# Performance work log

Measured on AMD Instinct MI355X. Metric: run time of the kernel, lower is better.

## Reference

```python
import jax, jax.numpy as jnp
import numpy as np

N = 40000   # nodes
E = 600000  # edges
G = 64      # graphs
DIN = 128   # input feature dim
H = 128     # hidden_channels
L = 3       # num_layers


def setup_inputs() -> dict:
    key = jax.random.key(0)
    ks = jax.random.split(key, 16)
    s = 0.05
    inp = {}
    inp["x"] = jax.random.normal(ks[0], (N, DIN), jnp.float32)
    inp["edge_attr"] = jax.random.normal(ks[1], (E,), jnp.float32)
    inp["node_w"] = jax.random.normal(ks[2], (DIN, H), jnp.float32) * s
    inp["node_b"] = jnp.zeros((H,), jnp.float32)
    inp["edge_w"] = jax.random.normal(ks[3], (1, H), jnp.float32) * s
    inp["edge_b"] = jnp.zeros((H,), jnp.float32)
    inp["t"] = jnp.ones((L,), jnp.float32)  # learn_t init 1.0
    inp["lin1_w"] = jax.random.normal(ks[4], (L, H, 2 * H), jnp.float32) * s
    inp["lin1_b"] = jnp.zeros((L, 2 * H), jnp.float32)
    inp["ln1_g"] = jnp.ones((L, 2 * H), jnp.float32)
    inp["ln1_bt"] = jnp.zeros((L, 2 * H), jnp.float32)
    inp["lin2_w"] = jax.random.normal(ks[5], (L, 2 * H, H), jnp.float32) * s
    inp["lin2_b"] = jnp.zeros((L, H), jnp.float32)
    inp["blk_g"] = jnp.ones((L, H), jnp.float32)
    inp["blk_b"] = jnp.zeros((L, H), jnp.float32)
    inp["hw1"] = jax.random.normal(ks[6], (H, H // 2), jnp.float32) * s
    inp["hb1"] = jnp.zeros((H // 2,), jnp.float32)
    inp["hw2"] = jax.random.normal(ks[7], (H // 2, H // 4), jnp.float32) * s
    inp["hb2"] = jnp.zeros((H // 4,), jnp.float32)
    inp["hw3"] = jax.random.normal(ks[8], (H // 4, 1), jnp.float32) * s
    inp["hb3"] = jnp.zeros((1,), jnp.float32)
    inp["edge_index"] = jax.random.randint(ks[9], (2, E), 0, N, jnp.int32)
    inp["batch"] = jnp.sort(jax.random.randint(ks[10], (N,), 0, G, jnp.int32))
    return inp


def _layer_norm(v, g, b):
    mu = jnp.mean(v, axis=-1, keepdims=True)
    var = jnp.var(v, axis=-1, keepdims=True)
    return (v - mu) * jax.lax.rsqrt(var + 1e-5) * g + b


def reference(x, edge_attr, node_w, node_b, edge_w, edge_b, t,
              lin1_w, lin1_b, ln1_g, ln1_bt, lin2_w, lin2_b,
              blk_g, blk_b, hw1, hb1, hw2, hb2, hw3, hb3,
              edge_index, batch):
    src, dst = edge_index[0], edge_index[1]
    h = x @ node_w + node_b                       # [N, H]
    ea = edge_attr[:, None] @ edge_w + edge_b     # [E, H]

    def genconv(xn, i):
        # message: relu(x_j + e) + eps
        msg = jax.nn.relu(xn[src] + ea) + 1e-7    # [E, H]
        # scatter-softmax over dst with learnable temperature t
        logit = msg * t[i]
        m = jax.ops.segment_max(logit, dst, num_segments=N)
        m = jnp.where(jnp.isfinite(m), m, 0.0)    # isolated nodes
        ex = jnp.exp(logit - m[dst])
        den = jax.ops.segment_sum(ex, dst, num_segments=N)
        agg = jax.ops.segment_sum(ex * msg, dst, num_segments=N) / jnp.maximum(den, 1e-16)
        o = agg + xn                              # add root
        # GENConv MLP: Linear(H,2H) -> LayerNorm -> ReLU -> Linear(2H,H)
        o = jax.nn.relu(_layer_norm(o @ lin1_w[i] + lin1_b[i], ln1_g[i], ln1_bt[i]))
        return o @ lin2_w[i] + lin2_b[i]

    # layer 0: bare conv (as in the torch forward)
    h = genconv(h, 0)
    # layers 1..L-1: DeepGCNLayer res+ (norm -> act -> [dropout=id in eval] -> conv -> residual)
    for i in range(1, L):
        r = jax.nn.relu(_layer_norm(h, blk_g[i], blk_b[i]))
        h = h + genconv(r, i)
    # final norm+act uses layer 0's norm/act
    h = jax.nn.relu(_layer_norm(h, blk_g[0], blk_b[0]))
    # global mean pool over graphs
    cnt = jax.ops.segment_sum(jnp.ones((N,), h.dtype), batch, num_segments=G)
    pooled = jax.ops.segment_sum(h, batch, num_segments=G) / jnp.maximum(cnt, 1.0)[:, None]
    # MLP head (dropout = identity in eval)
    o = jax.nn.relu(pooled @ hw1 + hb1)
    o = jax.nn.relu(o @ hw2 + hb2)
    return o @ hw3 + hb3                          # [G, 1]
```

## Files before the change

### kernel.cpp

```cpp
#include <hip/hip_runtime.h>
#include <math.h>

#define NN 40000
#define NE 600000
#define NG 64
#define DIM_IN 128
#define HH 128
#define HH2 256

using half8 = __attribute__((ext_vector_type(8))) _Float16;
using half4 = __attribute__((ext_vector_type(4))) _Float16;
using h2    = __attribute__((ext_vector_type(2))) _Float16;
using f4    = __attribute__((ext_vector_type(4))) float;

__device__ __forceinline__ int lower_bound_dev(const int* a, int n, int key) {
    int lo = 0, hi = n;
    while (lo < hi) { int mid = (lo + hi) >> 1; if (a[mid] < key) lo = mid + 1; else hi = mid; }
    return lo;
}

__global__ void convert_w_kernel(const float* __restrict__ node_w,
                                 const float* __restrict__ lin1_w, const float* __restrict__ lin2_w,
                                 _Float16* __restrict__ nwt,
                                 _Float16* __restrict__ w1t, _Float16* __restrict__ w2t)
{
    int id = blockIdx.x * blockDim.x + threadIdx.x;
    if (id < 16384) { int n = id >> 7, k = id & 127; nwt[id] = (_Float16)node_w[k*128 + n]; return; }
    id -= 16384;
    if (id < 98304) {
        int l = id >> 15, r = id & 32767;
        int n = r >> 7, k = r & 127;
        w1t[id] = (_Float16)lin1_w[l*32768 + k*256 + n];
        return;
    }
    id -= 98304;
    if (id < 98304) {
        int l = id >> 15, r = id & 32767;
        int n = r >> 8, k = r & 255;
        w2t[id] = (_Float16)lin2_w[l*32768 + k*128 + n];
    }
}

__global__ void count_rank_kernel(const int* __restrict__ dst, int* __restrict__ counts,
                                  int* __restrict__ rank) {
    int e = blockIdx.x * blockDim.x + threadIdx.x;
    if (e < NE) rank[e] = atomicAdd(&counts[dst[e]], 1);
}

__global__ __launch_bounds__(1024) void scanA_kernel(const int* __restrict__ counts,
                                                     int* __restrict__ tmp, int* __restrict__ btot) {
    __shared__ int wpre[16];
    int t = threadIdx.x, lane = t & 63, wid = t >> 6;
    int i = blockIdx.x * 1024 + t;
    int v = (i < NN) ? counts[i] : 0;
    int s = v;
    #pragma unroll
    for (int off = 1; off < 64; off <<= 1) {
        int u = __shfl_up(s, off, 64);
        if (lane >= off) s += u;
    }
    if (lane == 63) wpre[wid] = s;
    __syncthreads();
    if (t == 0) {
        int run = 0;
        #pragma unroll
        for (int j = 0; j < 16; ++j) { int xv = wpre[j]; wpre[j] = run; run += xv; }
        btot[blockIdx.x] = run;
    }
    __syncthreads();
    if (i < NN) tmp[i] = s + wpre[wid];
}

__global__ __launch_bounds__(64) void scanB_kernel(const int* __restrict__ btot,
                                                   int* __restrict__ boff, int nb) {
    int t = threadIdx.x;
    int v = (t < nb) ? btot[t] : 0;
    int s = v;
    #pragma unroll
    for (int off = 1; off < 64; off <<= 1) {
        int u = __shfl_up(s, off, 64);
        if (t >= off) s += u;
    }
    if (t < nb) boff[t] = s - v;
}

__global__ __launch_bounds__(1024) void scanC_kernel(const int* __restrict__ tmp,
                                                     const int* __restrict__ boff,
                                                     int* __restrict__ rowp) {
    int i = blockIdx.x * 1024 + threadIdx.x;
    if (i < NN) rowp[i + 1] = tmp[i] + boff[blockIdx.x];
    if (i == 0) rowp[0] = 0;
}

__global__ void fill2_kernel(const int* __restrict__ src, const int* __restrict__ dst,
                             const float* __restrict__ eattr, const int* __restrict__ rowp,
                             const int* __restrict__ rank, int2* __restrict__ rec) {
    int e = blockIdx.x * blockDim.x + threadIdx.x;
    if (e < NE) {
        int pos = rowp[dst[e]] + rank[e];
        rec[pos] = make_int2(src[e], __float_as_int(eattr[e]));
    }
}

__global__ __launch_bounds__(256) void agg_kernel(
    const _Float16* __restrict__ xh,
    const int* __restrict__ row_ptr,
    const int2* __restrict__ rec,
    const float* __restrict__ ew, const float* __restrict__ eb,
    const float* __restrict__ tptr, int layer,
    _Float16* __restrict__ oh)
{
    int d = blockIdx.x * 4 + (threadIdx.x >> 6);
    int lane = threadIdx.x & 63;
    int half = lane >> 5;
    int sl = lane & 31;
    int c0 = 4 * sl;
    float tc2 = tptr[layer] * 1.44269504f;
    float ewv[4], ebv[4];
    #pragma unroll
    for (int c = 0; c < 4; ++c) { ewv[c] = ew[c0 + c]; ebv[c] = eb[c0 + c]; }
    int beg = row_ptr[d], end = row_ptr[d + 1];
    float den[4] = {0.f, 0.f, 0.f, 0.f}, num[4] = {0.f, 0.f, 0.f, 0.f};
    for (int base = beg; base < end; base += 64) {
        int cnt = min(64, end - base);
        int2 mv = rec[base + min(lane, cnt - 1)];
        int sv = mv.x;
        float av = __int_as_float(mv.y);
        int pcnt = (cnt + 1) >> 1;
        half4 gA[4], gB[4]; float aA[4], aB[4];
        auto issue = [&](half4 (&g)[4], float (&aa)[4], int p0) {
            #pragma unroll
            for (int u = 0; u < 4; ++u) {
                int je = min(2 * (p0 + u) + half, cnt - 1);
                int s = __shfl(sv, je, 64);
                aa[u] = __shfl(av, je, 64);
                g[u] = *(const half4*)(xh + ((size_t)s << 7) + c0);
            }
        };
        auto consume = [&](half4 (&g)[4], float (&aa)[4], int p0) {
            #pragma unroll
            for (int u = 0; u < 4; ++u) {
                int je = 2 * (p0 + u) + half;
                if (je < cnt) {
                    #pragma unroll
                    for (int c = 0; c < 4; ++c) {
                        float r = fmaxf(__fmaf_rn(aa[u], ewv[c], ebv[c]) + (float)g[u][c], 0.f);
                        float e = exp2f(r * tc2);
                        den[c] += e;
                        num[c] = __fmaf_rn(e, r, num[c]);
                    }
                }
            }
        };
        issue(gA, aA, 0);
        for (int p0 = 0; p0 < pcnt; p0 += 8) {
            if (p0 + 4 < pcnt) issue(gB, aB, p0 + 4);
            consume(gA, aA, p0);
            if (p0 + 8 < pcnt) issue(gA, aA, p0 + 8);
            if (p0 + 4 < pcnt) consume(gB, aB, p0 + 4);
        }
    }
    #pragma unroll
    for (int c = 0; c < 4; ++c) {
        den[c] += __shfl_xor(den[c], 32, 64);
        num[c] += __shfl_xor(num[c], 32, 64);
    }
    if (half == 0) {
        half4 sv4 = *(const half4*)(xh + ((size_t)d << 7) + c0);
        half4 ov;
        #pragma unroll
        for (int c = 0; c < 4; ++c) {
            float o = num[c] / fmaxf(den[c], 1e-16f) + 1e-7f + (float)sv4[c];
            ov[c] = (_Float16)o;
        }
        *(half4*)(oh + ((size_t)d << 7) + c0) = ov;
    }
}

__global__ __launch_bounds__(256) void gemm_mfma(
    const float* __restrict__ A, const _Float16* __restrict__ Bt,
    const float* __restrict__ bias, _Float16* __restrict__ C,
    int M, int N, int K)
{
    constexpr int LDA = 40;
    __shared__ _Float16 As[64 * LDA];
    __shared__ _Float16 Bs[128 * LDA];
    int t = threadIdx.x;
    int row0 = blockIdx.y * 64;
    int col0 = blockIdx.x * 128;
    int w = t >> 6, lane = t & 63;
    int wm = w & 1, wn = w >> 1;
    int q = lane >> 4, l16 = lane & 15;
    f4 acc[2][4];
    #pragma unroll
    for (int i = 0; i < 2; ++i)
        #pragma unroll
        for (int j = 0; j < 4; ++j)
            acc[i][j] = (f4){0.f, 0.f, 0.f, 0.f};

    for (int k0 = 0; k0 < K; k0 += 32) {
        #pragma unroll
        for (int p = 0; p < 2; ++p) {
            int idx = t + p * 256;
            int r = idx >> 3, seg = idx & 7;
            float4 v = *(const float4*)(A + (size_t)(row0 + r) * K + k0 + seg * 4);
            half4 o; o.x = (_Float16)v.x; o.y = (_Float16)v.y; o.z = (_Float16)v.z; o.w = (_Float16)v.w;
            *(half4*)&As[r * LDA + seg * 4] = o;
        }
        #pragma unroll
        for (int i = 0; i < 2; ++i) {
            int idx = t + i * 256;
            int r = idx >> 2, seg = idx & 3;
            *(float4*)&Bs[r * LDA + seg * 8] =
                *(const float4*)(Bt + (size_t)(col0 + r) * K + k0 + seg * 8);
        }
        __syncthreads();
        half8 af[2], bf[4];
        #pragma unroll
        for (int i = 0; i < 2; ++i)
            af[i] = *(const half8*)&As[(wm * 32 + i * 16 + l16) * LDA + q * 8];
        #pragma unroll
        for (int j = 0; j < 4; ++j)
            bf[j] = *(const half8*)&Bs[(wn * 64 + j * 16 + l16) * LDA + q * 8];
        #pragma unroll
        for (int i = 0; i < 2; ++i)
            #pragma unroll
            for (int j = 0; j < 4; ++j)
                acc[i][j] = __builtin_amdgcn_mfma_f32_16x16x32_f16(af[i], bf[j], acc[i][j], 0, 0, 0);
        __syncthreads();
    }
    #pragma unroll
    for (int j = 0; j < 4; ++j) {
        int col = col0 + wn * 64 + j * 16 + l16;
        float bv = bias[col];
        #pragma unroll
        for (int i = 0; i < 2; ++i) {
            int rbase = row0 + wm * 32 + i * 16 + q * 4;
            #pragma unroll
            for (int rg = 0; rg < 4; ++rg)
                C[(size_t)(rbase + rg) * N + col] = (_Float16)(acc[i][j][rg] + bv);
        }
    }
}

template<int RES, int FINAL>
__global__ __launch_bounds__(256) void mlp_fused(
    const _Float16* __restrict__ Ain,
    const _Float16* __restrict__ w1t,
    const float* __restrict__ b1,
    const float* __restrict__ g1, const float* __restrict__ bt1,
    const _Float16* __restrict__ w2t,
    const float* __restrict__ b2,
    float* __restrict__ h,
    const float* __restrict__ bg, const float* __restrict__ bb,
    _Float16* __restrict__ xout)
{
    constexpr int LDA = 136;
    constexpr int LDB = 40;
    constexpr int LDM = 264;
    __shared__ _Float16 As[64 * LDA];
    __shared__ _Float16 Bs[256 * LDB];
    __shared__ _Float16 midh[64 * LDM];
    __shared__ float ssum[64][2], ssum2[64][2];
    int t = threadIdx.x;
    int row0 = blockIdx.x * 64;
    int w = t >> 6, lane = t & 63;
    int wm = w & 1, wn = w >> 1;
    int q = lane >> 4, l16 = lane & 15;

    #pragma unroll
    for (int p = 0; p < 4; ++p) {
        int idx = t + p * 256;
        int r = idx >> 4, seg = idx & 15;
        *(float4*)&As[r * LDA + seg * 8] =
            *(const float4*)(Ain + (size_t)(row0 + r) * 128 + seg * 8);
    }

    f4 acc[2][8];
    #pragma unroll
    for (int i = 0; i < 2; ++i)
        #pragma unroll
        for (int j = 0; j < 8; ++j)
            acc[i][j] = (f4){0.f, 0.f, 0.f, 0.f};
    for (int k0 = 0; k0 < 128; k0 += 32) {
        #pragma unroll
        for (int p = 0; p < 4; ++p) {
            int idx = t + p * 256;
            int r = idx >> 2, seg = idx & 3;
            *(float4*)&Bs[r * LDB + seg * 8] =
                *(const float4*)(w1t + (size_t)r * 128 + k0 + seg * 8);
        }
        __syncthreads();
        half8 af[2], bf[8];
        #pragma unroll
        for (int i = 0; i < 2; ++i)
            af[i] = *(const half8*)&As[(wm * 32 + i * 16 + l16) * LDA + k0 + q * 8];
        #pragma unroll
        for (int j = 0; j < 8; ++j)
            bf[j] = *(const half8*)&Bs[(wn * 128 + j * 16 + l16) * LDB + q * 8];
        #pragma unroll
        for (int i = 0; i < 2; ++i)
            #pragma unroll
            for (int j = 0; j < 8; ++j)
                acc[i][j] = __builtin_amdgcn_mfma_f32_16x16x32_f16(af[i], bf[j], acc[i][j], 0, 0, 0);
        __syncthreads();
    }

    float b1v[8], g1v[8], bt1v[8];
    #pragma unroll
    for (int j = 0; j < 8; ++j) {
        int col = wn * 128 + j * 16 + l16;
        b1v[j] = b1[col]; g1v[j] = g1[col]; bt1v[j] = bt1[col];
    }
    float vals[2][8][4];
    #pragma unroll
    for (int i = 0; i < 2; ++i)
        #pragma unroll
        for (int j = 0; j < 8; ++j)
            #pragma unroll
            for (int rg = 0; rg < 4; ++rg)
                vals[i][j][rg] = acc[i][j][rg] + b1v[j];
    #pragma unroll
    for (int i = 0; i < 2; ++i) {
        #pragma unroll
        for (int rg = 0; rg < 4; ++rg) {
            float ps = 0.f, ps2 = 0.f;
            #pragma unroll
            for (int j = 0; j < 8; ++j) { float v = vals[i][j][rg]; ps += v; ps2 += v * v; }
            #pragma unroll
            for (int off = 1; off < 16; off <<= 1) {
                ps  += __shfl_xor(ps,  off, 16);
                ps2 += __shfl_xor(ps2, off, 16);
            }
            if (l16 == 0) {
                int row = wm * 32 + i * 16 + q * 4 + rg;
                ssum[row][wn] = ps; ssum2[row][wn] = ps2;
            }
        }
    }
    __syncthreads();
    #pragma unroll
    for (int i = 0; i < 2; ++i) {
        #pragma unroll
        for (int rg = 0; rg < 4; ++rg) {
            int row = wm * 32 + i * 16 + q * 4 + rg;
            float S = ssum[row][0] + ssum[row][1];
            float S2 = ssum2[row][0] + ssum2[row][1];
            float mu = S * (1.0f / 256.0f);
            float var = S2 * (1.0f / 256.0f) - mu * mu;
            float rstd = rsqrtf(var + 1e-5f);
            #pragma unroll
            for (int j = 0; j < 8; ++j) {
                int col = wn * 128 + j * 16 + l16;
                float o = fmaxf((vals[i][j][rg] - mu) * rstd * g1v[j] + bt1v[j], 0.f);
                midh[row * LDM + col] = (_Float16)o;
            }
        }
    }
    __syncthreads();

    f4 acc2[2][4];
    #pragma unroll
    for (int i = 0; i < 2; ++i)
        #pragma unroll
        for (int j = 0; j < 4; ++j)
            acc2[i][j] = (f4){0.f, 0.f, 0.f, 0.f};
    for (int k0 = 0; k0 < 256; k0 += 32) {
        #pragma unroll
        for (int p = 0; p < 2; ++p) {
            int idx = t + p * 256;
            int r = idx >> 2, seg = idx & 3;
            *(float4*)&Bs[r * LDB + seg * 8] =
                *(const float4*)(w2t + (size_t)r * 256 + k0 + seg * 8);
        }
        __syncthreads();
        half8 af2[2], bf2[4];
        #pragma unroll
        for (int i = 0; i < 2; ++i)
            af2[i] = *(const half8*)&midh[(wm * 32 + i * 16 + l16) * LDM + k0 + q * 8];
        #pragma unroll
        for (int j = 0; j < 4; ++j)
            bf2[j] = *(const half8*)&Bs[(wn * 64 + j * 16 + l16) * LDB + q * 8];
        #pragma unroll
        for (int i = 0; i < 2; ++i)
            #pragma unroll
            for (int j = 0; j < 4; ++j)
                acc2[i][j] = __builtin_amdgcn_mfma_f32_16x16x32_f16(af2[i], bf2[j], acc2[i][j], 0, 0, 0);
        __syncthreads();
    }

    float b2v[4], bgv[4], bbv[4];
    #pragma unroll
    for (int j = 0; j < 4; ++j) {
        int col = wn * 64 + j * 16 + l16;
        b2v[j] = b2[col]; bgv[j] = bg[col]; bbv[j] = bb[col];
    }
    float ov[2][4][4];
    #pragma unroll
    for (int i = 0; i < 2; ++i) {
        #pragma unroll
        for (int rg = 0; rg < 4; ++rg) {
            int row = wm * 32 + i * 16 + q * 4 + rg;
            #pragma unroll
            for (int j = 0; j < 4; ++j) {
                int col = wn * 64 + j * 16 + l16;
                float v = acc2[i][j][rg] + b2v[j];
                size_t gidx = (size_t)(row0 + row) * 128 + col;
                if (RES) v += h[gidx];
                if (!FINAL) h[gidx] = v;
                ov[i][j][rg] = v;
            }
        }
    }
    #pragma unroll
    for (int i = 0; i < 2; ++i) {
        #pragma unroll
        for (int rg = 0; rg < 4; ++rg) {
            float ps = 0.f, ps2 = 0.f;
            #pragma unroll
            for (int j = 0; j < 4; ++j) { float v = ov[i][j][rg]; ps += v; ps2 += v * v; }
            #pragma unroll
            for (int off = 1; off < 16; off <<= 1) {
                ps  += __shfl_xor(ps,  off, 16);
                ps2 += __shfl_xor(ps2, off, 16);
            }
            if (l16 == 0) {
                int row = wm * 32 + i * 16 + q * 4 + rg;
                ssum[row][wn] = ps; ssum2[row][wn] = ps2;
            }
        }
    }
    __syncthreads();
    #pragma unroll
    for (int i = 0; i < 2; ++i) {
        #pragma unroll
        for (int rg = 0; rg < 4; ++rg) {
            int row = wm * 32 + i * 16 + q * 4 + rg;
            float S = ssum[row][0] + ssum[row][1];
            float S2 = ssum2[row][0] + ssum2[row][1];
            float mu = S * (1.0f / 128.0f);
            float var = S2 * (1.0f / 128.0f) - mu * mu;
            float rstd = rsqrtf(var + 1e-5f);
            #pragma unroll
            for (int j = 0; j < 4; ++j) {
                int col = wn * 64 + j * 16 + l16;
                float o = fmaxf((ov[i][j][rg] - mu) * rstd * bgv[j] + bbv[j], 0.f);
                xout[(size_t)(row0 + row) * 128 + col] = (_Float16)o;
            }
        }
    }
}

__global__ __launch_bounds__(128) void pool_kernel(
    const _Float16* __restrict__ f, const int* __restrict__ batch, float* __restrict__ pooled)
{
    int g = blockIdx.x;
    int chunk = blockIdx.y;
    int c = threadIdx.x;
    int s = lower_bound_dev(batch, NN, g);
    int e = lower_bound_dev(batch, NN, g + 1);
    int len = e - s;
    if (len <= 0) return;
    int nch = gridDim.y;
    int per = (len + nch - 1) / nch;
    int cs = s + chunk * per;
    int ce = min(cs + per, e);
    if (cs >= ce) return;
    float acc = 0.f;
    for (int n = cs; n < ce; ++n) acc += (float)f[(size_t)n * HH + c];
    atomicAdd(&pooled[g * HH + c], acc);
}

__global__ __launch_bounds__(128) void head_kernel(
    const float* __restrict__ pooled, const int* __restrict__ batch,
    const float* __restrict__ hw1, const float* __restrict__ hb1,
    const float* __restrict__ hw2, const float* __restrict__ hb2,
    const float* __restrict__ hw3, const float* __restrict__ hb3,
    float* __restrict__ out)
{
    __shared__ float p[HH];
    __shared__ float o1[64];
    __shared__ float o2[32];
    int g = blockIdx.x;
    int t = threadIdx.x;
    int s = lower_bound_dev(batch, NN, g);
    int e = lower_bound_dev(batch, NN, g + 1);
    float cnt = fmaxf((float)(e - s), 1.0f);
    p[t] = pooled[g * HH + t] / cnt;
    __syncthreads();
    if (t < 64) {
        float acc = hb1[t];
        for (int k = 0; k < HH; ++k) acc += p[k] * hw1[k * 64 + t];
        o1[t] = fmaxf(acc, 0.f);
    }
    __syncthreads();
    if (t < 32) {
        float acc = hb2[t];
        for (int k = 0; k < 64; ++k) acc += o1[k] * hw2[k * 32 + t];
        o2[t] = fmaxf(acc, 0.f);
    }
    __syncthreads();
    if (t == 0) {
        float acc = hb3[0];
        for (int k = 0; k < 32; ++k) acc += o2[k] * hw3[k];
        out[g] = acc;
    }
}

extern "C" void kernel_launch(void* const* d_in, const int* in_sizes, int n_in,
                              void* d_out, int out_size, void* d_ws, size_t ws_size,
                              hipStream_t stream)
{
    const float* x      = (const float*)d_in[0];
    const float* eattr  = (const float*)d_in[1];
    const float* node_w = (const float*)d_in[2];
    const float* node_b = (const float*)d_in[3];
    const float* edge_w = (const float*)d_in[4];
    const float* edge_b = (const float*)d_in[5];
    const float* tptr   = (const float*)d_in[6];
    const float* lin1_w = (const float*)d_in[7];
    const float* lin1_b = (const float*)d_in[8];
    const float* ln1_g  = (const float*)d_in[9];
    const float* ln1_bt = (const float*)d_in[10];
    const float* lin2_w = (const float*)d_in[11];
    const float* lin2_b = (const float*)d_in[12];
    const float* blk_g  = (const float*)d_in[13];
    const float* blk_b  = (const float*)d_in[14];
    const float* hw1    = (const float*)d_in[15];
    const float* hb1    = (const float*)d_in[16];
    const float* hw2    = (const float*)d_in[17];
    const float* hb2    = (const float*)d_in[18];
    const float* hw3    = (const float*)d_in[19];
    const float* hb3    = (const float*)d_in[20];
    const int*   eidx   = (const int*)d_in[21];
    const int*   batch  = (const int*)d_in[22];
    const int* src = eidx;
    const int* dst = eidx + NE;
    float* out = (float*)d_out;

    char* ws = (char*)d_ws;
    size_t off = 0;
    auto carve = [&](size_t bytes) -> char* {
        char* p = ws + off;
        off = (off + bytes + 255) & ~(size_t)255;
        return p;
    };
    float*    h      = (float*)carve((size_t)NN * HH * 4);
    _Float16* xnh    = (_Float16*)carve((size_t)NN * HH * 2);
    _Float16* oh     = (_Float16*)carve((size_t)NN * HH * 2);
    _Float16* rh     = (_Float16*)carve((size_t)NN * HH * 2);
    _Float16* nwt    = (_Float16*)carve((size_t)16384 * 2);
    _Float16* w1t    = (_Float16*)carve((size_t)98304 * 2);
    _Float16* w2t    = (_Float16*)carve((size_t)98304 * 2);
    int*      counts = (int*)carve((size_t)NN * 4);
    int*      rank   = (int*)carve((size_t)NE * 4);
    int*      tmp    = (int*)carve((size_t)NN * 4);
    int*      btot   = (int*)carve((size_t)64 * 4);
    int*      boff   = (int*)carve((size_t)64 * 4);
    int*      rowp   = (int*)carve((size_t)(NN + 1) * 4);
    int2*     rec    = (int2*)carve((size_t)NE * 8);
    float*    pooled = (float*)carve((size_t)NG * HH * 4);

    hipMemsetAsync(counts, 0, (size_t)NN * 4, stream);
    hipMemsetAsync(pooled, 0, (size_t)NG * HH * 4, stream);

    {
        int total = 16384 + 98304 + 98304;
        convert_w_kernel<<<(total + 255) / 256, 256, 0, stream>>>(
            node_w, lin1_w, lin2_w, nwt, w1t, w2t);
    }
    const int NB = (NN + 1023) / 1024;
    count_rank_kernel<<<(NE + 255) / 256, 256, 0, stream>>>(dst, counts, rank);
    scanA_kernel<<<NB, 1024, 0, stream>>>(counts, tmp, btot);
    scanB_kernel<<<1, 64, 0, stream>>>(btot, boff, NB);
    scanC_kernel<<<NB, 1024, 0, stream>>>(tmp, boff, rowp);
    fill2_kernel<<<(NE + 255) / 256, 256, 0, stream>>>(src, dst, eattr, rowp, rank, rec);

    gemm_mfma<<<dim3(1, NN / 64), 256, 0, stream>>>(x, nwt, node_b, xnh, NN, HH, DIM_IN);

    agg_kernel<<<NN / 4, 256, 0, stream>>>(xnh, rowp, rec, edge_w, edge_b, tptr, 0, oh);
    mlp_fused<0, 0><<<NN / 64, 256, 0, stream>>>(
        oh, w1t, lin1_b, ln1_g, ln1_bt, w2t, lin2_b,
        h, blk_g + 1 * HH, blk_b + 1 * HH, xnh);
    agg_kernel<<<NN / 4, 256, 0, stream>>>(xnh, rowp, rec, edge_w, edge_b, tptr, 1, oh);
    mlp_fused<1, 0><<<NN / 64, 256, 0, stream>>>(
        oh, w1t + 32768, lin1_b + HH2, ln1_g + HH2, ln1_bt + HH2, w2t + 32768, lin2_b + HH,
        h, blk_g + 2 * HH, blk_b + 2 * HH, xnh);
    agg_kernel<<<NN / 4, 256, 0, stream>>>(xnh, rowp, rec, edge_w, edge_b, tptr, 2, oh);
    mlp_fused<1, 1><<<NN / 64, 256, 0, stream>>>(
        oh, w1t + 2 * 32768, lin1_b + 2 * HH2, ln1_g + 2 * HH2, ln1_bt + 2 * HH2,
        w2t + 2 * 32768, lin2_b + 2 * HH,
        h, blk_g, blk_b, rh);

    pool_kernel<<<dim3(NG, 8), 128, 0, stream>>>(rh, batch, pooled);
    head_kernel<<<NG, 128, 0, stream>>>(pooled, batch, hw1, hb1, hw2, hb2, hw3, hb3, out);
}
```

Baseline: 402.6 us.

## Widen aggregation gathers to half8 with packed fp16 math; read GEMM weights directly

The aggregation kernel now has each 16-lane group gather 8 halves per lane, so four edges are processed per wave step. It computes the edge message with packed fp16 arithmetic and uses a bias trick instead of branches to mask padded edges. Each wave now handles two destination nodes, which halves the grid. The node-embedding GEMM and the fused MLP drop their LDS staging of weights and the per-k syncthreads, loading B fragments straight from global memory (relying on cache), and the A tile is loaded once in full. The risks are fp16 precision in the message computation and more global-load traffic for the weights.

```diff
diff --git a/kernel.cpp b/kernel.cpp
--- a/kernel.cpp
+++ b/kernel.cpp
@@ -110,128 +110,139 @@
     const float* __restrict__ tptr, int layer,
     _Float16* __restrict__ oh)
 {
-    int d = blockIdx.x * 4 + (threadIdx.x >> 6);
+    int wid = threadIdx.x >> 6;
     int lane = threadIdx.x & 63;
-    int half = lane >> 5;
-    int sl = lane & 31;
-    int c0 = 4 * sl;
+    int grp = lane >> 4;
+    int sl = lane & 15;
+    int c0 = 8 * sl;
     float tc2 = tptr[layer] * 1.44269504f;
-    float ewv[4], ebv[4];
-    #pragma unroll
-    for (int c = 0; c < 4; ++c) { ewv[c] = ew[c0 + c]; ebv[c] = eb[c0 + c]; }
-    int beg = row_ptr[d], end = row_ptr[d + 1];
-    float den[4] = {0.f, 0.f, 0.f, 0.f}, num[4] = {0.f, 0.f, 0.f, 0.f};
-    for (int base = beg; base < end; base += 64) {
-        int cnt = min(64, end - base);
-        int2 mv = rec[base + min(lane, cnt - 1)];
-        int sv = mv.x;
-        float av = __int_as_float(mv.y);
-        int pcnt = (cnt + 1) >> 1;
-        half4 gA[4], gB[4]; float aA[4], aB[4];
-        auto issue = [&](half4 (&g)[4], float (&aa)[4], int p0) {
-            #pragma unroll
-            for (int u = 0; u < 4; ++u) {
-                int je = min(2 * (p0 + u) + half, cnt - 1);
-                int s = __shfl(sv, je, 64);
-                aa[u] = __shfl(av, je, 64);
-                g[u] = *(const half4*)(xh + ((size_t)s << 7) + c0);
-            }
-        };
-        auto consume = [&](half4 (&g)[4], float (&aa)[4], int p0) {
-            #pragma unroll
-            for (int u = 0; u < 4; ++u) {
-                int je = 2 * (p0 + u) + half;
-                if (je < cnt) {
-                    #pragma unroll
-                    for (int c = 0; c < 4; ++c) {
-                        float r = fmaxf(__fmaf_rn(aa[u], ewv[c], ebv[c]) + (float)g[u][c], 0.f);
-                        float e = exp2f(r * tc2);
-                        den[c] += e;
-                        num[c] = __fmaf_rn(e, r, num[c]);
+    h2 ew2[4], eb2[4];
+    #pragma unroll
+    for (int k = 0; k < 4; ++k) {
+        h2 tw; tw.x = (_Float16)ew[c0 + 2*k]; tw.y = (_Float16)ew[c0 + 2*k + 1]; ew2[k] = tw;
+        h2 tb; tb.x = (_Float16)eb[c0 + 2*k]; tb.y = (_Float16)eb[c0 + 2*k + 1]; eb2[k] = tb;
+    }
+    int d0 = blockIdx.x * 4 + wid;
+    #pragma unroll
+    for (int rr = 0; rr < 2; ++rr) {
+        int d = d0 + rr * (NN / 2);
+        int beg = row_ptr[d], end = row_ptr[d + 1];
+        float den[8], num[8];
+        #pragma unroll
+        for (int c = 0; c < 8; ++c) { den[c] = 0.f; num[c] = 0.f; }
+        for (int base = beg; base < end; base += 64) {
+            int cnt = min(64, end - base);
+            int2 mv = rec[base + min(lane, cnt - 1)];
+            int sv = mv.x;
+            float av = __int_as_float(mv.y);
+            int qcnt = (cnt + 3) >> 2;
+            half8 gA[4], gB[4]; h2 aA[4], aB[4]; float bA[4], bB[4];
+            auto issue = [&](half8 (&g)[4], h2 (&a2)[4], float (&bn)[4], int u0) {
+                #pragma unroll
+                for (int v = 0; v < 4; ++v) {
+                    if (u0 + v < qcnt) {
+                        int idx = 4 * (u0 + v) + grp;
+                        int s = __shfl(sv, idx, 64);
+                        float a = __shfl(av, idx, 64);
+                        g[v] = *(const half8*)(xh + ((size_t)(unsigned)s << 7) + c0);
+                        _Float16 ah = (_Float16)a;
+                        h2 t2; t2.x = ah; t2.y = ah; a2[v] = t2;
+                        bn[v] = (idx < cnt) ? 0.f : -1e4f;
                     }
                 }
-            }
-        };
-        issue(gA, aA, 0);
-        for (int p0 = 0; p0 < pcnt; p0 += 8) {
-            if (p0 + 4 < pcnt) issue(gB, aB, p0 + 4);
-            consume(gA, aA, p0);
-            if (p0 + 8 < pcnt) issue(gA, aA, p0 + 8);
-            if (p0 + 4 < pcnt) consume(gB, aB, p0 + 4);
-        }
-    }
-    #pragma unroll
-    for (int c = 0; c < 4; ++c) {
-        den[c] += __shfl_xor(den[c], 32, 64);
-        num[c] += __shfl_xor(num[c], 32, 64);
-    }
-    if (half == 0) {
-        half4 sv4 = *(const half4*)(xh + ((size_t)d << 7) + c0);
-        half4 ov;
-        #pragma unroll
-        for (int c = 0; c < 4; ++c) {
-            float o = num[c] / fmaxf(den[c], 1e-16f) + 1e-7f + (float)sv4[c];
-            ov[c] = (_Float16)o;
-        }
-        *(half4*)(oh + ((size_t)d << 7) + c0) = ov;
+            };
+            auto consume = [&](half8 (&g)[4], h2 (&a2)[4], float (&bn)[4], int u0) {
+                #pragma unroll
+                for (int v = 0; v < 4; ++v) {
+                    if (u0 + v < qcnt) {
+                        #pragma unroll
+                        for (int k = 0; k < 4; ++k) {
+                            h2 z = a2[v] * ew2[k] + eb2[k];
+                            h2 x2; x2.x = g[v][2*k]; x2.y = g[v][2*k+1];
+                            z = z + x2;
+                            float r0 = fmaxf((float)z.x, 0.f);
+                            float r1 = fmaxf((float)z.y, 0.f);
+                            float e0 = exp2f(__fmaf_rn(r0, tc2, bn[v]));
+                            float e1 = exp2f(__fmaf_rn(r1, tc2, bn[v]));
+                            den[2*k]   += e0; num[2*k]   = __fmaf_rn(e0, r0, num[2*k]);
+                            den[2*k+1] += e1; num[2*k+1] = __fmaf_rn(e1, r1, num[2*k+1]);
+                        }
+                    }
+                }
+            };
+            issue(gA, aA, bA, 0);
+            for (int u0 = 0; u0 < qcnt; u0 += 8) {
+                if (u0 + 4 < qcnt) issue(gB, aB, bB, u0 + 4);
+                consume(gA, aA, bA, u0);
+                if (u0 + 8 < qcnt) issue(gA, aA, bA, u0 + 8);
+                if (u0 + 4 < qcnt) consume(gB, aB, bB, u0 + 4);
+            }
+        }
+        #pragma unroll
+        for (int c = 0; c < 8; ++c) {
+            den[c] += __shfl_xor(den[c], 16, 64);
+            num[c] += __shfl_xor(num[c], 16, 64);
+            den[c] += __shfl_xor(den[c], 32, 64);
+            num[c] += __shfl_xor(num[c], 32, 64);
+        }
+        if (grp == 0) {
+            half8 s8 = *(const half8*)(xh + ((size_t)d << 7) + c0);
+            half8 ov;
+            #pragma unroll
+            for (int c = 0; c < 8; ++c) {
+                float o = num[c] / fmaxf(den[c], 1e-16f) + 1e-7f + (float)s8[c];
+                ov[c] = (_Float16)o;
+            }
+            *(half8*)(oh + ((size_t)d << 7) + c0) = ov;
+        }
     }
 }
 
 __global__ __launch_bounds__(256) void gemm_mfma(
     const float* __restrict__ A, const _Float16* __restrict__ Bt,
-    const float* __restrict__ bias, _Float16* __restrict__ C,
-    int M, int N, int K)
-{
-    constexpr int LDA = 40;
+    const float* __restrict__ bias, _Float16* __restrict__ C)
+{
+    constexpr int K = 128, N = 128;
+    constexpr int LDA = 136;
     __shared__ _Float16 As[64 * LDA];
-    __shared__ _Float16 Bs[128 * LDA];
     int t = threadIdx.x;
-    int row0 = blockIdx.y * 64;
-    int col0 = blockIdx.x * 128;
+    int row0 = blockIdx.x * 64;
     int w = t >> 6, lane = t & 63;
     int wm = w & 1, wn = w >> 1;
     int q = lane >> 4, l16 = lane & 15;
+    #pragma unroll
+    for (int p = 0; p < 8; ++p) {
+        int idx = t + p * 256;
+        int r = idx >> 5, seg = idx & 31;
+        float4 v = *(const float4*)(A + (size_t)(row0 + r) * K + seg * 4);
+        half4 o; o.x = (_Float16)v.x; o.y = (_Float16)v.y; o.z = (_Float16)v.z; o.w = (_Float16)v.w;
+        *(half4*)&As[r * LDA + seg * 4] = o;
+    }
+    __syncthreads();
     f4 acc[2][4];
     #pragma unroll
     for (int i = 0; i < 2; ++i)
         #pragma unroll
         for (int j = 0; j < 4; ++j)
             acc[i][j] = (f4){0.f, 0.f, 0.f, 0.f};
-
+    #pragma unroll
     for (int k0 = 0; k0 < K; k0 += 32) {
-        #pragma unroll
-        for (int p = 0; p < 2; ++p) {
-            int idx = t + p * 256;
-            int r = idx >> 3, seg = idx & 7;
-            float4 v = *(const float4*)(A + (size_t)(row0 + r) * K + k0 + seg * 4);
-            half4 o; o.x = (_Float16)v.x; o.y = (_Float16)v.y; o.z = (_Float16)v.z; o.w = (_Float16)v.w;
-            *(half4*)&As[r * LDA + seg * 4] = o;
-        }
-        #pragma unroll
-        for (int i = 0; i < 2; ++i) {
-            int idx = t + i * 256;
-            int r = idx >> 2, seg = idx & 3;
-            *(float4*)&Bs[r * LDA + seg * 8] =
-                *(const float4*)(Bt + (size_t)(col0 + r) * K + k0 + seg * 8);
-        }
-        __syncthreads();
         half8 af[2], bf[4];
         #pragma unroll
         for (int i = 0; i < 2; ++i)
-            af[i] = *(const half8*)&As[(wm * 32 + i * 16 + l16) * LDA + q * 8];
+            af[i] = *(const half8*)&As[(wm * 32 + i * 16 + l16) * LDA + k0 + q * 8];
         #pragma unroll
         for (int j = 0; j < 4; ++j)
-            bf[j] = *(const half8*)&Bs[(wn * 64 + j * 16 + l16) * LDA + q * 8];
+            bf[j] = *(const half8*)(Bt + (size_t)(wn * 64 + j * 16 + l16) * K + k0 + q * 8);
         #pragma unroll
         for (int i = 0; i < 2; ++i)
             #pragma unroll
             for (int j = 0; j < 4; ++j)
                 acc[i][j] = __builtin_amdgcn_mfma_f32_16x16x32_f16(af[i], bf[j], acc[i][j], 0, 0, 0);
-        __syncthreads();
     }
     #pragma unroll
     for (int j = 0; j < 4; ++j) {
-        int col = col0 + wn * 64 + j * 16 + l16;
+        int col = wn * 64 + j * 16 + l16;
         float bv = bias[col];
         #pragma unroll
         for (int i = 0; i < 2; ++i) {
@@ -256,10 +267,8 @@
     _Float16* __restrict__ xout)
 {
     constexpr int LDA = 136;
-    constexpr int LDB = 40;
     constexpr int LDM = 264;
     __shared__ _Float16 As[64 * LDA];
-    __shared__ _Float16 Bs[256 * LDB];
     __shared__ _Float16 midh[64 * LDM];
     __shared__ float ssum[64][2], ssum2[64][2];
     int t = threadIdx.x;
@@ -275,6 +284,7 @@
         *(float4*)&As[r * LDA + seg * 8] =
             *(const float4*)(Ain + (size_t)(row0 + r) * 128 + seg * 8);
     }
+    __syncthreads();
 
     f4 acc[2][8];
     #pragma unroll
@@ -282,28 +292,20 @@
         #pragma unroll
         for (int j = 0; j < 8; ++j)
             acc[i][j] = (f4){0.f, 0.f, 0.f, 0.f};
+    #pragma unroll
     for (int k0 = 0; k0 < 128; k0 += 32) {
-        #pragma unroll
-        for (int p = 0; p < 4; ++p) {
-            int idx = t + p * 256;
-            int r = idx >> 2, seg = idx & 3;
-            *(float4*)&Bs[r * LDB + seg * 8] =
-                *(const float4*)(w1t + (size_t)r * 128 + k0 + seg * 8);
-        }
-        __syncthreads();
         half8 af[2], bf[8];
         #pragma unroll
         for (int i = 0; i < 2; ++i)
             af[i] = *(const half8*)&As[(wm * 32 + i * 16 + l16) * LDA + k0 + q * 8];
         #pragma unroll
         for (int j = 0; j < 8; ++j)
-            bf[j] = *(const half8*)&Bs[(wn * 128 + j * 16 + l16) * LDB + q * 8];
+            bf[j] = *(const half8*)(w1t + (size_t)(wn * 128 + j * 16 + l16) * 128 + k0 + q * 8);
         #pragma unroll
         for (int i = 0; i < 2; ++i)
             #pragma unroll
             for (int j = 0; j < 8; ++j)
                 acc[i][j] = __builtin_amdgcn_mfma_f32_16x16x32_f16(af[i], bf[j], acc[i][j], 0, 0, 0);
-        __syncthreads();
     }
 
     float b1v[8], g1v[8], bt1v[8];
@@ -365,28 +367,20 @@
         #pragma unroll
         for (int j = 0; j < 4; ++j)
             acc2[i][j] = (f4){0.f, 0.f, 0.f, 0.f};
+    #pragma unroll
     for (int k0 = 0; k0 < 256; k0 += 32) {
-        #pragma unroll
-        for (int p = 0; p < 2; ++p) {
-            int idx = t + p * 256;
-            int r = idx >> 2, seg = idx & 3;
-            *(float4*)&Bs[r * LDB + seg * 8] =
-                *(const float4*)(w2t + (size_t)r * 256 + k0 + seg * 8);
-        }
-        __syncthreads();
         half8 af2[2], bf2[4];
         #pragma unroll
         for (int i = 0; i < 2; ++i)
             af2[i] = *(const half8*)&midh[(wm * 32 + i * 16 + l16) * LDM + k0 + q * 8];
         #pragma unroll
         for (int j = 0; j < 4; ++j)
-            bf2[j] = *(const half8*)&Bs[(wn * 64 + j * 16 + l16) * LDB + q * 8];
+            bf2[j] = *(const half8*)(w2t + (size_t)(wn * 64 + j * 16 + l16) * 256 + k0 + q * 8);
         #pragma unroll
         for (int i = 0; i < 2; ++i)
             #pragma unroll
             for (int j = 0; j < 4; ++j)
                 acc2[i][j] = __builtin_amdgcn_mfma_f32_16x16x32_f16(af2[i], bf2[j], acc2[i][j], 0, 0, 0);
-        __syncthreads();
     }
 
     float b2v[4], bgv[4], bbv[4];
@@ -576,17 +570,17 @@
     scanC_kernel<<<NB, 1024, 0, stream>>>(tmp, boff, rowp);
     fill2_kernel<<<(NE + 255) / 256, 256, 0, stream>>>(src, dst, eattr, rowp, rank, rec);
 
-    gemm_mfma<<<dim3(1, NN / 64), 256, 0, stream>>>(x, nwt, node_b, xnh, NN, HH, DIM_IN);
-
-    agg_kernel<<<NN / 4, 256, 0, stream>>>(xnh, rowp, rec, edge_w, edge_b, tptr, 0, oh);
+    gemm_mfma<<<NN / 64, 256, 0, stream>>>(x, nwt, node_b, xnh);
+
+    agg_kernel<<<NN / 8, 256, 0, stream>>>(xnh, rowp, rec, edge_w, edge_b, tptr, 0, oh);
     mlp_fused<0, 0><<<NN / 64, 256, 0, stream>>>(
         oh, w1t, lin1_b, ln1_g, ln1_bt, w2t, lin2_b,
         h, blk_g + 1 * HH, blk_b + 1 * HH, xnh);
-    agg_kernel<<<NN / 4, 256, 0, stream>>>(xnh, rowp, rec, edge_w, edge_b, tptr, 1, oh);
+    agg_kernel<<<NN / 8, 256, 0, stream>>>(xnh, rowp, rec, edge_w, edge_b, tptr, 1, oh);
     mlp_fused<1, 0><<<NN / 64, 256, 0, stream>>>(
         oh, w1t + 32768, lin1_b + HH2, ln1_g + HH2, ln1_bt + HH2, w2t + 32768, lin2_b + HH,
         h, blk_g + 2 * HH, blk_b + 2 * HH, xnh);
-    agg_kernel<<<NN / 4, 256, 0, stream>>>(xnh, rowp, rec, edge_w, edge_b, tptr, 2, oh);
+    agg_kernel<<<NN / 8, 256, 0, stream>>>(xnh, rowp, rec, edge_w, edge_b, tptr, 2, oh);
     mlp_fused<1, 1><<<NN / 64, 256, 0, stream>>>(
         oh, w1t + 2 * 32768, lin1_b + 2 * HH2, ln1_g + 2 * HH2, ln1_bt + 2 * HH2,
         w2t + 2 * 32768, lin2_b + 2 * HH,
```

New measurement: 474.5 us. 1.18x slower.

## Split aggregation per node across two wavefronts by channel half, prescale by t

Applied to the files above, without the earlier changes.

Each destination node's aggregation is now split across two wavefronts, each covering 64 channels, so every lane handles 2 channels instead of 4. The grid doubles to give more parallelism and fewer registers per lane. The edge weight and bias are prescaled by t·log2(e), which removes a multiply per element, and the numerator is rescaled once at the end. In exchange, the rec records and row pointers are read twice per node, and the gathers shrink to 4-byte loads, which may lower memory efficiency.

```diff
diff --git a/kernel.cpp b/kernel.cpp
--- a/kernel.cpp
+++ b/kernel.cpp
@@ -110,45 +110,47 @@
     const float* __restrict__ tptr, int layer,
     _Float16* __restrict__ oh)
 {
-    int d = blockIdx.x * 4 + (threadIdx.x >> 6);
+    int task = blockIdx.x * 4 + (threadIdx.x >> 6);
+    int d = task >> 1;
+    int ch0 = (task & 1) << 6;
     int lane = threadIdx.x & 63;
     int half = lane >> 5;
     int sl = lane & 31;
-    int c0 = 4 * sl;
+    int c0 = ch0 + 2 * sl;
     float tc2 = tptr[layer] * 1.44269504f;
-    float ewv[4], ebv[4];
-    #pragma unroll
-    for (int c = 0; c < 4; ++c) { ewv[c] = ew[c0 + c]; ebv[c] = eb[c0 + c]; }
+    float itc = 1.0f / tc2;
+    float ew0 = ew[c0] * tc2,     eb0 = eb[c0] * tc2;
+    float ew1 = ew[c0 + 1] * tc2, eb1 = eb[c0 + 1] * tc2;
     int beg = row_ptr[d], end = row_ptr[d + 1];
-    float den[4] = {0.f, 0.f, 0.f, 0.f}, num[4] = {0.f, 0.f, 0.f, 0.f};
+    float den0 = 0.f, num0 = 0.f, den1 = 0.f, num1 = 0.f;
     for (int base = beg; base < end; base += 64) {
         int cnt = min(64, end - base);
         int2 mv = rec[base + min(lane, cnt - 1)];
         int sv = mv.x;
         float av = __int_as_float(mv.y);
         int pcnt = (cnt + 1) >> 1;
-        half4 gA[4], gB[4]; float aA[4], aB[4];
-        auto issue = [&](half4 (&g)[4], float (&aa)[4], int p0) {
+        h2 gA[4], gB[4]; float aA[4], aB[4];
+        auto issue = [&](h2 (&g)[4], float (&aa)[4], int p0) {
             #pragma unroll
             for (int u = 0; u < 4; ++u) {
                 int je = min(2 * (p0 + u) + half, cnt - 1);
                 int s = __shfl(sv, je, 64);
                 aa[u] = __shfl(av, je, 64);
-                g[u] = *(const half4*)(xh + ((size_t)s << 7) + c0);
+                g[u] = *(const h2*)(xh + ((size_t)s << 7) + c0);
             }
         };
-        auto consume = [&](half4 (&g)[4], float (&aa)[4], int p0) {
+        auto consume = [&](h2 (&g)[4], float (&aa)[4], int p0) {
             #pragma unroll
             for (int u = 0; u < 4; ++u) {
                 int je = 2 * (p0 + u) + half;
                 if (je < cnt) {
-                    #pragma unroll
-                    for (int c = 0; c < 4; ++c) {
-                        float r = fmaxf(__fmaf_rn(aa[u], ewv[c], ebv[c]) + (float)g[u][c], 0.f);
-                        float e = exp2f(r * tc2);
-                        den[c] += e;
-                        num[c] = __fmaf_rn(e, r, num[c]);
-                    }
+                    float p0v = __fmaf_rn(aa[u], ew0, eb0);
+                    float p1v = __fmaf_rn(aa[u], ew1, eb1);
+                    float r0 = fmaxf(__fmaf_rn((float)g[u].x, tc2, p0v), 0.f);
+                    float r1 = fmaxf(__fmaf_rn((float)g[u].y, tc2, p1v), 0.f);
+                    float e0 = exp2f(r0), e1 = exp2f(r1);
+                    den0 += e0; num0 = __fmaf_rn(e0, r0, num0);
+                    den1 += e1; num1 = __fmaf_rn(e1, r1, num1);
                 }
             }
         };
@@ -160,20 +162,14 @@
             if (p0 + 4 < pcnt) consume(gB, aB, p0 + 4);
         }
     }
-    #pragma unroll
-    for (int c = 0; c < 4; ++c) {
-        den[c] += __shfl_xor(den[c], 32, 64);
-        num[c] += __shfl_xor(num[c], 32, 64);
-    }
+    den0 += __shfl_xor(den0, 32, 64); num0 += __shfl_xor(num0, 32, 64);
+    den1 += __shfl_xor(den1, 32, 64); num1 += __shfl_xor(num1, 32, 64);
     if (half == 0) {
-        half4 sv4 = *(const half4*)(xh + ((size_t)d << 7) + c0);
-        half4 ov;
-        #pragma unroll
-        for (int c = 0; c < 4; ++c) {
-            float o = num[c] / fmaxf(den[c], 1e-16f) + 1e-7f + (float)sv4[c];
-            ov[c] = (_Float16)o;
-        }
-        *(half4*)(oh + ((size_t)d << 7) + c0) = ov;
+        h2 s2 = *(const h2*)(xh + ((size_t)d << 7) + c0);
+        float o0 = num0 * itc / fmaxf(den0, 1e-16f) + 1e-7f + (float)s2.x;
+        float o1 = num1 * itc / fmaxf(den1, 1e-16f) + 1e-7f + (float)s2.y;
+        h2 ov; ov.x = (_Float16)o0; ov.y = (_Float16)o1;
+        *(h2*)(oh + ((size_t)d << 7) + c0) = ov;
     }
 }
 
@@ -578,15 +574,15 @@
 
     gemm_mfma<<<dim3(1, NN / 64), 256, 0, stream>>>(x, nwt, node_b, xnh, NN, HH, DIM_IN);
 
-    agg_kernel<<<NN / 4, 256, 0, stream>>>(xnh, rowp, rec, edge_w, edge_b, tptr, 0, oh);
+    agg_kernel<<<NN / 2, 256, 0, stream>>>(xnh, rowp, rec, edge_w, edge_b, tptr, 0, oh);
     mlp_fused<0, 0><<<NN / 64, 256, 0, stream>>>(
         oh, w1t, lin1_b, ln1_g, ln1_bt, w2t, lin2_b,
         h, blk_g + 1 * HH, blk_b + 1 * HH, xnh);
-    agg_kernel<<<NN / 4, 256, 0, stream>>>(xnh, rowp, rec, edge_w, edge_b, tptr, 1, oh);
+    agg_kernel<<<NN / 2, 256, 0, stream>>>(xnh, rowp, rec, edge_w, edge_b, tptr, 1, oh);
     mlp_fused<1, 0><<<NN / 64, 256, 0, stream>>>(
         oh, w1t + 32768, lin1_b + HH2, ln1_g + HH2, ln1_bt + HH2, w2t + 32768, lin2_b + HH,
         h, blk_g + 2 * HH, blk_b + 2 * HH, xnh);
-    agg_kernel<<<NN / 4, 256, 0, stream>>>(xnh, rowp, rec, edge_w, edge_b, tptr, 2, oh);
+    agg_kernel<<<NN / 2, 256, 0, stream>>>(xnh, rowp, rec, edge_w, edge_b, tptr, 2, oh);
     mlp_fused<1, 1><<<NN / 64, 256, 0, stream>>>(
         oh, w1t + 2 * 32768, lin1_b + 2 * HH2, ln1_g + 2 * HH2, ln1_bt + 2 * HH2,
         w2t + 2 * 32768, lin2_b + 2 * HH,
```

Result: slower. 423.9 us (+5.3%).
